# Performance work log

Hardware: AMD Instinct MI355X
Metric: run time of the kernel (lower is better)

## Reference

```python
import jax, jax.numpy as jnp
import numpy as np

K = 9
VOCAB = 7
DIM = 512
LOW = 256  # downsampled bottleneck dim
N_LAYERS = 2
EPS = 1e-5


def _inorm(x, g, b):
    # InstanceNorm1d over length axis (biased var), x: (N, C, K)
    m = jnp.mean(x, axis=-1, keepdims=True)
    v = jnp.mean((x - m) ** 2, axis=-1, keepdims=True)
    return g[None, :, None] * (x - m) * jax.lax.rsqrt(v + EPS) + b[None, :, None]


def _conv5_same(x, w, b):
    # x: (N, C, K), w: (O, C, 5), dilation 1, padding 'same' -> pad 2
    y = jax.lax.conv_general_dilated(
        x, w, window_strides=(1,), padding=[(2, 2)],
        dimension_numbers=('NCH', 'OIH', 'NCH'))
    return y + b[None, :, None]


def _bytenet_layer(x, p):
    (g1, b1, g2, b2, g3, b3, w1, c1b, w2, c2b, w3, c3b) = p
    h = jax.nn.gelu(_inorm(x, g1, b1), approximate=False)
    h = jnp.einsum('nck,oc->nok', h, w1) + c1b[None, :, None]      # 1x1 conv 512->256
    h = jax.nn.gelu(_inorm(h, g2, b2), approximate=False)
    h = _conv5_same(h, w2, c2b)                                     # k=5 conv 256->256
    h = jax.nn.gelu(_inorm(h, g3, b3), approximate=False)
    h = jnp.einsum('nck,oc->nok', h, w3) + c3b[None, :, None]      # 1x1 conv 256->512
    return h + x  # dropout is identity in eval


def setup_inputs() -> dict:
    key = jax.random.key(0)
    ks = jax.random.split(key, 16)
    x = jax.random.randint(ks[0], (8, 2048), 0, VOCAB)
    emb = jax.random.normal(ks[1], (VOCAB, DIM), jnp.float32) * 0.02
    emb = emb.at[6].set(0.0)  # padding_idx=6
    d = {
        'x': x,
        'emb': emb,
        'ln1_w': jnp.ones((N_LAYERS, DIM)), 'ln1_b': jnp.zeros((N_LAYERS, DIM)),
        'ln2_w': jnp.ones((N_LAYERS, LOW)), 'ln2_b': jnp.zeros((N_LAYERS, LOW)),
        'ln3_w': jnp.ones((N_LAYERS, LOW)), 'ln3_b': jnp.zeros((N_LAYERS, LOW)),
        'c1_w': jax.random.normal(ks[2], (N_LAYERS, LOW, DIM), jnp.float32) * 0.02,
        'c1_b': jnp.zeros((N_LAYERS, LOW)),
        'c2_w': jax.random.normal(ks[3], (N_LAYERS, LOW, LOW, 5), jnp.float32) * 0.02,
        'c2_b': jnp.zeros((N_LAYERS, LOW)),
        'c3_w': jax.random.normal(ks[4], (N_LAYERS, DIM, LOW), jnp.float32) * 0.02,
        'c3_b': jnp.zeros((N_LAYERS, DIM)),
        'out_w': jax.random.normal(ks[5], (VOCAB, DIM * K), jnp.float32) * 0.02,
        'out_b': jnp.zeros((VOCAB,)),
    }
    return d


def reference(x, emb, ln1_w, ln1_b, ln2_w, ln2_b, ln3_w, ln3_b,
              c1_w, c1_b, c2_w, c2_b, c3_w, c3_b, out_w, out_b):
    B, L = x.shape
    W = L - K + 1
    e = emb[x]                                        # (B, L, D)
    idx = jnp.arange(W)[:, None] + jnp.arange(K)      # (W, K)
    win = e[:, idx, :]                                # (B, W, K, D)
    h = win.transpose(0, 1, 3, 2).reshape(B * W, DIM, K)  # (N, D, K)
    for i in range(N_LAYERS):
        p = (ln1_w[i], ln1_b[i], ln2_w[i], ln2_b[i], ln3_w[i], ln3_b[i],
             c1_w[i], c1_b[i], c2_w[i], c2_b[i], c3_w[i], c3_b[i])
        h = _bytenet_layer(h, p)
    pred = h.reshape(B * W, DIM * K) @ out_w.T + out_b
    return pred.reshape(B, W, VOCAB)
```

## Files before the change

kernel.cpp:

```cpp
#include <hip/hip_runtime.h>

typedef __attribute__((ext_vector_type(8))) short bfv8;
typedef __attribute__((ext_vector_type(4))) float f32x4;
typedef __attribute__((ext_vector_type(4))) unsigned short usv4;

typedef __attribute__((address_space(1))) const void gvoid;
typedef __attribute__((address_space(3))) void lvoid;
__device__ __forceinline__ void gload16(const void* g, void* l) {
  __builtin_amdgcn_global_load_lds((gvoid*)g, (lvoid*)l, 16, 0, 0);
}

__device__ __forceinline__ float bf2f(unsigned short u) {
  union { unsigned int i; float f; } c; c.i = ((unsigned int)u) << 16; return c.f;
}
__device__ __forceinline__ unsigned short f2bf(float f) {
  union { float f; unsigned int i; } c; c.f = f;
  unsigned int r = c.i + 0x7FFFu + ((c.i >> 16) & 1u);
  return (unsigned short)(r >> 16);
}
__device__ __forceinline__ float gelu_(float x) {
  float z2 = 1.5957691216057308f * x * __builtin_fmaf(0.044715f, x * x, 1.0f);
  float e = __expf(z2);
  float t = __builtin_amdgcn_rcpf(e + 1.0f);
  return x - x * t;
}
__device__ __forceinline__ int div9(int col) {
  return (int)(__umulhi((unsigned)col, 954437177u) >> 1);
}

#define CHP 132
#define CHP2 66

__global__ void k_prep(const float* c1w, const float* c2w, const float* c3w,
                       const float* outw, unsigned short* W1b, unsigned short* W2t,
                       unsigned short* W3b, float* OWt) {
  int i = blockIdx.x * 256 + threadIdx.x;
  if (i < 262144) { W1b[i] = f2bf(c1w[i]); return; }
  i -= 262144;
  if (i < 655360) {
    int ii = i & 255, o = (i >> 8) & 255, rest = i >> 16;
    int t = rest % 5, l = rest / 5;
    W2t[i] = f2bf(c2w[(((l * 256 + o) << 8) + ii) * 5 + t]);
    return;
  }
  i -= 655360;
  if (i < 262144) { W3b[i] = f2bf(c3w[i]); return; }
  i -= 262144;
  if (i < 32256) {
    int c = i & 511, rk = i >> 9;
    int r = rk / 9, k = rk - 9 * r;
    OWt[i] = outw[r * 4608 + c * 9 + k];
  }
}

__global__ void k_x0(const int* x, const float* emb, unsigned short* X, int n0) {
  int idx = blockIdx.x * 256 + threadIdx.x;
  int c4 = idx & 127, nl = idx >> 7;
  int gn = n0 + nl, b = gn >> 11, w = gn & 2047;
  unsigned short* dst = X + (size_t)(12 + nl * 12) * 512 + (c4 << 2);
  const int* xb = x + (b << 11);
  #pragma unroll
  for (int k = 0; k < 9; k++) {
    int t = w + k; if (t > 2047) t = 2047;
    const float* e = emb + xb[t] * 512 + (c4 << 2);
    float4 ev = *(const float4*)e;
    usv4 pk;
    pk[0] = f2bf(ev.x); pk[1] = f2bf(ev.y);
    pk[2] = f2bf(ev.z); pk[3] = f2bf(ev.w);
    *(usv4*)(dst + k * 512) = pk;
  }
}

__global__ void k_zpad(unsigned short* AL) {
  int i = threadIdx.x;
  for (; i < 12 * 256; i += 256) AL[i] = 0;
}

template <int MODE>
__global__ __launch_bounds__(512, 2) void k_gemm(
    const unsigned short* __restrict__ Aw, const unsigned short* __restrict__ Bsrc,
    const float* __restrict__ n1w, const float* __restrict__ n1b,
    const float* __restrict__ gw, const float* __restrict__ gb,
    unsigned short* __restrict__ Out, int nkc) {
  __shared__ __align__(16) unsigned short smem[69632];
  unsigned short* sE = smem;

  const int KROW = (MODE == 0) ? 512 : 256;
  const int KSTEPS = (MODE == 1) ? 20 : 8;
  int tid = threadIdx.x, wv = tid >> 6, ln = tid & 63;
  int lr = ln >> 3, lu = ln & 7;
  int swz = (lu ^ lr) << 3;
  int w0 = blockIdx.x << 5;
  int col0 = blockIdx.x * 288;

  int brow[5];
  #pragma unroll
  for (int s = 0; s < 5; s++) {
    int colg = col0 + (s << 6) + (wv << 3) + lr;
    if (colg >= nkc) colg = nkc - 1;
    brow[s] = colg + 3 * div9(colg) + 12;
  }

  f32x4 acc[4][9];
  #pragma unroll
  for (int i = 0; i < 4; i++)
    #pragma unroll
    for (int j = 0; j < 9; j++) acc[i][j] = (f32x4){0.f, 0.f, 0.f, 0.f};

  auto stage = [&](int buf, int ks) {
    int kb, dlt; const unsigned short* Ab;
    if (MODE == 1) {
      int t = ks % 5; kb = (ks / 5) << 6; dlt = t - 2; Ab = Aw + t * 65536;
    } else { kb = ks << 6; dlt = 0; Ab = Aw; }
    unsigned short* cA = smem + buf * 16384;
    unsigned short* cB = smem + 32768 + buf * 18432;
    #pragma unroll
    for (int p = 0; p < 4; p++) {
      int m = (p << 6) + (wv << 3) + lr;
      gload16(Ab + (size_t)m * KROW + kb + swz, cA + (p << 12) + (wv << 9));
    }
    #pragma unroll
    for (int s = 0; s < 4; s++)
      gload16(Bsrc + (size_t)(brow[s] + dlt) * KROW + kb + swz,
              cB + (s << 12) + (wv << 9));
    if (wv < 4)
      gload16(Bsrc + (size_t)(brow[4] + dlt) * KROW + kb + swz,
              cB + (4 << 12) + (wv << 9));
  };

  stage(0, 0);
  __syncthreads();

  int cur = 0;
  for (int ks = 0; ks < KSTEPS; ks++) {
    unsigned short* cA = smem + cur * 16384;
    unsigned short* cB = smem + 32768 + cur * 18432;

    if (MODE == 0) {
      int cg = tid & 15, win = tid >> 4;
      int u = cg >> 1, sub = (cg & 1) << 3;
      int gch = (ks << 6) + (cg << 2);
      float v[9][4], s1[4] = {0.f, 0.f, 0.f, 0.f};
      #pragma unroll
      for (int k = 0; k < 9; k++) {
        int cl = win * 9 + k;
        usv4 rv = *(const usv4*)((char*)cB + cl * 128 + ((u ^ (cl & 7)) << 4) + sub);
        #pragma unroll
        for (int j = 0; j < 4; j++) { v[k][j] = bf2f(rv[j]); s1[j] += v[k][j]; }
      }
      float mn[4], rr[4], gg[4], bo[4];
      #pragma unroll
      for (int j = 0; j < 4; j++) {
        mn[j] = s1[j] * (1.0f / 9.0f);
        float q = 0.f;
        #pragma unroll
        for (int k = 0; k < 9; k++) { float d = v[k][j] - mn[j]; q += d * d; }
        rr[j] = rsqrtf(q * (1.0f / 9.0f) + 1e-5f);
        gg[j] = n1w[gch + j]; bo[j] = n1b[gch + j];
      }
      #pragma unroll
      for (int k = 0; k < 9; k++) {
        int cl = win * 9 + k;
        usv4 pk;
        #pragma unroll
        for (int j = 0; j < 4; j++)
          pk[j] = f2bf(gelu_(gg[j] * (v[k][j] - mn[j]) * rr[j] + bo[j]));
        *(usv4*)((char*)cB + cl * 128 + ((u ^ (cl & 7)) << 4) + sub) = pk;
      }
      __syncthreads();
    }

    if (ks + 1 < KSTEPS) stage(cur ^ 1, ks + 1);

    int l16 = ln & 15, loct = ln >> 4;
    int wm = wv >> 1, wn = wv & 1;
    #pragma unroll
    for (int kk = 0; kk < 2; kk++) {
      int kbyte = (kk << 6) + (loct << 4);
      bfv8 af[4], bf_[9];
      #pragma unroll
      for (int mi = 0; mi < 4; mi++) {
        int row = (wm << 6) + (mi << 4) + l16;
        af[mi] = *(const bfv8*)((const char*)cA + row * 128 + (kbyte ^ ((row & 7) << 4)));
      }
      #pragma unroll
      for (int ni = 0; ni < 9; ni++) {
        int row = wn * 144 + (ni << 4) + l16;
        bf_[ni] = *(const bfv8*)((const char*)cB + row * 128 + (kbyte ^ ((row & 7) << 4)));
      }
      #pragma unroll
      for (int mi = 0; mi < 4; mi++)
        #pragma unroll
        for (int ni = 0; ni < 9; ni++)
          acc[mi][ni] = __builtin_amdgcn_mfma_f32_16x16x32_bf16(
              af[mi], bf_[ni], acc[mi][ni], 0, 0, 0);
    }
    __syncthreads();
    cur ^= 1;
  }

  int l16 = ln & 15, loct = ln >> 4;
  #pragma unroll
  for (int R = 0; R < 2; R++) {
    if (R) __syncthreads();
    if ((wv >> 2) == R) {
      int chh = (((wv >> 1) & 1) << 6) + (loct << 2);
      int colb = (wv & 1) * 144 + l16;
      #pragma unroll
      for (int mi = 0; mi < 4; mi++) {
        #pragma unroll
        for (int ni = 0; ni < 9; ni++) {
          usv4 pk;
          #pragma unroll
          for (int q = 0; q < 4; q++) pk[q] = f2bf(acc[mi][ni][q]);
          *(usv4*)(sE + (colb + (ni << 4)) * CHP + chh + (mi << 4)) = pk;
        }
      }
    }
    __syncthreads();
    #pragma unroll
    for (int tt = 0; tt < 2; tt++) {
      int t = tid + tt * 512;
      int c4 = t & 31, win = t >> 5;
      int chl = (R << 7) + (c4 << 2);
      const unsigned short* sb = sE + (win * 9) * CHP + (c4 << 2);
      size_t ob = (size_t)(12 + (size_t)(w0 + win) * 12) * 256 + chl;
      float s1[4] = {0.f, 0.f, 0.f, 0.f}, s2[4] = {0.f, 0.f, 0.f, 0.f};
      #pragma unroll
      for (int k = 0; k < 9; k++) {
        usv4 rv = *(const usv4*)(sb + k * CHP);
        #pragma unroll
        for (int j = 0; j < 4; j++) {
          float f = bf2f(rv[j]);
          s1[j] += f; s2[j] = __builtin_fmaf(f, f, s2[j]);
        }
      }
      float mn[4], rr[4], gg[4], bo[4];
      #pragma unroll
      for (int j = 0; j < 4; j++) {
        mn[j] = s1[j] * (1.0f / 9.0f);
        float var = s2[j] * (1.0f / 9.0f) - mn[j] * mn[j];
        rr[j] = rsqrtf(var + 1e-5f);
        gg[j] = gw[chl + j]; bo[j] = gb[chl + j];
      }
      #pragma unroll
      for (int k = 0; k < 9; k++) {
        usv4 rv = *(const usv4*)(sb + k * CHP);
        usv4 pk;
        #pragma unroll
        for (int j = 0; j < 4; j++)
          pk[j] = f2bf(gelu_(gg[j] * (bf2f(rv[j]) - mn[j]) * rr[j] + bo[j]));
        *(usv4*)(Out + ob + k * 256) = pk;
      }
      if (MODE == 0) {
        usv4 z = (usv4){0, 0, 0, 0};
        *(usv4*)(Out + ob + 9 * 256) = z;
        *(usv4*)(Out + ob + 10 * 256) = z;
        *(usv4*)(Out + ob + 11 * 256) = z;
      }
    }
  }
}

__global__ __launch_bounds__(256, 2) void k_gemm2(
    const unsigned short* __restrict__ Aw, const unsigned short* __restrict__ Bsrc,
    const float* __restrict__ cbias, unsigned short* __restrict__ Out, int nkc) {
  __shared__ __align__(16) unsigned short smem[34816];
  unsigned short* sE = smem;

  const int KROW = 256, KSTEPS = 4;
  int tid = threadIdx.x, wv = tid >> 6, ln = tid & 63;
  int lr = ln >> 3, lu = ln & 7;
  int swz = (lu ^ lr) << 3;
  int id = blockIdx.x;
  int slab = (id >> 3) & 3;
  int tile = ((id >> 5) << 3) | (id & 7);
  int m0 = slab << 7;
  int w0 = tile << 4;
  int col0 = tile * 144;

  int brow[5];
  #pragma unroll
  for (int s = 0; s < 5; s++) {
    int cl = (s < 4) ? ((s << 5) + (wv << 3) + lr) : (128 + (wv << 3) + lr);
    int colg = col0 + cl;
    if (colg >= nkc) colg = nkc - 1;
    brow[s] = colg + 3 * div9(colg) + 12;
  }
  const unsigned short* A0 = Aw + (size_t)m0 * KROW;

  f32x4 acc[2][9];
  #pragma unroll
  for (int i = 0; i < 2; i++)
    #pragma unroll
    for (int j = 0; j < 9; j++) acc[i][j] = (f32x4){0.f, 0.f, 0.f, 0.f};

  auto stage = [&](int buf, int ks) {
    int kb = ks << 6;
    unsigned short* cA = smem + buf * 8192;
    unsigned short* cB = smem + 16384 + buf * 9216;
    #pragma unroll
    for (int p = 0; p < 4; p++) {
      int m = (p << 5) + (wv << 3) + lr;
      gload16(A0 + (size_t)m * KROW + kb + swz, cA + ((p << 5) + (wv << 3)) * 64);
    }
    #pragma unroll
    for (int s = 0; s < 4; s++)
      gload16(Bsrc + (size_t)brow[s] * KROW + kb + swz,
              cB + ((s << 5) + (wv << 3)) * 64);
    if (wv < 2)
      gload16(Bsrc + (size_t)brow[4] * KROW + kb + swz,
              cB + (128 + (wv << 3)) * 64);
  };

  stage(0, 0);
  __syncthreads();

  int cur = 0;
  for (int ks = 0; ks < KSTEPS; ks++) {
    unsigned short* cA = smem + cur * 8192;
    unsigned short* cB = smem + 16384 + cur * 9216;
    if (ks + 1 < KSTEPS) stage(cur ^ 1, ks + 1);

    int l16 = ln & 15, loct = ln >> 4;
    #pragma unroll
    for (int kk = 0; kk < 2; kk++) {
      int kbyte = (kk << 6) + (loct << 4);
      bfv8 af[2], bf_[9];
      #pragma unroll
      for (int mi = 0; mi < 2; mi++) {
        int row = (wv << 5) + (mi << 4) + l16;
        af[mi] = *(const bfv8*)((const char*)cA + row * 128 + (kbyte ^ ((row & 7) << 4)));
      }
      #pragma unroll
      for (int ni = 0; ni < 9; ni++) {
        int row = (ni << 4) + l16;
        bf_[ni] = *(const bfv8*)((const char*)cB + row * 128 + (kbyte ^ ((row & 7) << 4)));
      }
      #pragma unroll
      for (int mi = 0; mi < 2; mi++)
        #pragma unroll
        for (int ni = 0; ni < 9; ni++)
          acc[mi][ni] = __builtin_amdgcn_mfma_f32_16x16x32_bf16(
              af[mi], bf_[ni], acc[mi][ni], 0, 0, 0);
    }
    __syncthreads();
    cur ^= 1;
  }

  int l16 = ln & 15, loct = ln >> 4;
  int c4 = tid & 15, win = tid >> 4;
  #pragma unroll
  for (int R = 0; R < 2; R++) {
    if (R) __syncthreads();
    if ((wv >> 1) == R) {
      int chh = ((wv & 1) << 5) + (loct << 2);
      #pragma unroll
      for (int mi = 0; mi < 2; mi++) {
        #pragma unroll
        for (int ni = 0; ni < 9; ni++) {
          usv4 pk;
          #pragma unroll
          for (int q = 0; q < 4; q++) pk[q] = f2bf(acc[mi][ni][q]);
          *(usv4*)(sE + ((ni << 4) + l16) * CHP2 + chh + (mi << 4)) = pk;
        }
      }
    }
    __syncthreads();
    {
      int chg = m0 + (R << 6) + (c4 << 2);
      const unsigned short* sb = sE + (win * 9) * CHP2 + (c4 << 2);
      size_t ob = (size_t)(12 + (size_t)(w0 + win) * 12) * 512 + chg;
      float cb[4];
      #pragma unroll
      for (int j = 0; j < 4; j++) cb[j] = cbias[chg + j];
      #pragma unroll
      for (int k = 0; k < 9; k++) {
        usv4 rv = *(const usv4*)(sb + k * CHP2);
        usv4 old = *(usv4*)(Out + ob + k * 512);
        usv4 pk;
        #pragma unroll
        for (int j = 0; j < 4; j++)
          pk[j] = f2bf(bf2f(rv[j]) + cb[j] + bf2f(old[j]));
        *(usv4*)(Out + ob + k * 512) = pk;
      }
    }
  }
}

__global__ void k_out(const unsigned short* X, const float* OWt, const float* outb,
                      float* pred, int n0, int nc) {
  int gw = (blockIdx.x * 256 + threadIdx.x) >> 6;
  int ln = threadIdx.x & 63;
  if (gw >= nc) return;
  int gn = n0 + gw, b = gn >> 11, w = gn & 2047;
  if (w >= 2040) return;
  const unsigned short* xb = X + (size_t)(12 + gw * 12) * 512 + ln * 8;
  float a[7];
  #pragma unroll
  for (int r = 0; r < 7; r++) a[r] = 0.f;
  for (int k = 0; k < 9; k++) {
    bfv8 xv = *(const bfv8*)(xb + k * 512);
    float xf[8];
    #pragma unroll
    for (int j = 0; j < 8; j++) xf[j] = bf2f((unsigned short)xv[j]);
    #pragma unroll
    for (int r = 0; r < 7; r++) {
      const float* wp = OWt + (r * 9 + k) * 512 + ln * 8;
      float4 w0 = *(const float4*)(wp);
      float4 w1 = *(const float4*)(wp + 4);
      a[r] += xf[0] * w0.x + xf[1] * w0.y + xf[2] * w0.z + xf[3] * w0.w +
              xf[4] * w1.x + xf[5] * w1.y + xf[6] * w1.z + xf[7] * w1.w;
    }
  }
  #pragma unroll
  for (int r = 0; r < 7; r++)
    for (int off = 32; off; off >>= 1) a[r] += __shfl_down(a[r], off);
  if (ln == 0) {
    float* o = pred + (size_t)(b * 2040 + w) * 7;
    #pragma unroll
    for (int r = 0; r < 7; r++) o[r] = a[r] + outb[r];
  }
}

extern "C" void kernel_launch(void* const* d_in, const int* in_sizes, int n_in,
                              void* d_out, int out_size, void* d_ws, size_t ws_size,
                              hipStream_t stream) {
  const int*   x    = (const int*)d_in[0];
  const float* emb  = (const float*)d_in[1];
  const float* ln1w = (const float*)d_in[2];
  const float* ln1b = (const float*)d_in[3];
  const float* ln2w = (const float*)d_in[4];
  const float* ln2b = (const float*)d_in[5];
  const float* ln3w = (const float*)d_in[6];
  const float* ln3b = (const float*)d_in[7];
  const float* c1w  = (const float*)d_in[8];
  const float* c2w  = (const float*)d_in[10];
  const float* c3w  = (const float*)d_in[12];
  const float* c3b  = (const float*)d_in[13];
  const float* outw = (const float*)d_in[14];
  const float* outb = (const float*)d_in[15];
  float* pred = (float*)d_out;

  int nc = 8192;
  while (nc > 128 &&
         2488320ull + (unsigned long long)(nc + 1) * 24576ull > ws_size)
    nc >>= 1;
  int nkc = nc * 9;
  int tiles288 = nc >> 5;
  int tiles144 = nc >> 4;
  int nchunks = 16384 / nc;

  char* ws = (char*)d_ws;
  unsigned short* W1b = (unsigned short*)(ws);
  unsigned short* W2t = (unsigned short*)(ws + 524288);
  unsigned short* W3b = (unsigned short*)(ws + 1835008);
  float*          OWt = (float*)(ws + 2359296);
  char* act = ws + 2488320;
  size_t hiB = (size_t)(nc + 1) * 12288;
  size_t loB = (size_t)(nc + 1) * 6144;
  unsigned short* X   = (unsigned short*)(act);
  unsigned short* AL  = (unsigned short*)(act + hiB);
  unsigned short* AL2 = (unsigned short*)(act + hiB + loB);

  k_prep<<<(1211904 + 255) / 256, 256, 0, stream>>>(c1w, c2w, c3w, outw,
                                                    W1b, W2t, W3b, OWt);
  k_zpad<<<1, 256, 0, stream>>>(AL);

  for (int ch = 0; ch < nchunks; ch++) {
    int n0 = ch * nc;
    k_x0<<<nc / 2, 256, 0, stream>>>(x, emb, X, n0);
    for (int l = 0; l < 2; l++) {
      k_gemm<0><<<dim3(tiles288, 1), 512, 0, stream>>>(
          W1b + l * 131072, X, ln1w + l * 512, ln1b + l * 512,
          ln2w + l * 256, ln2b + l * 256, AL, nkc);
      k_gemm<1><<<dim3(tiles288, 1), 512, 0, stream>>>(
          W2t + l * 327680, AL, nullptr, nullptr,
          ln3w + l * 256, ln3b + l * 256, AL2, nkc);
      k_gemm2<<<tiles144 * 4, 256, 0, stream>>>(
          W3b + l * 131072, AL2, c3b + l * 512, X, nkc);
    }
    k_out<<<nc / 4, 256, 0, stream>>>(X, OWt, outb, pred, n0, nc);
  }
}
```

Measured before the change: 774.5 us.

## Move first-norm GELU out of GEMM into producer epilogues writing a separate buffer

The instance-norm plus GELU on the 512-channel input is no longer done inside the first 1x1-conv GEMM's k-loop. It is now done once by the producer: the embedding kernel for layer 0, and the residual epilogue of the previous layer's output GEMM for layer 1. The results go to a new bf16 buffer T. This removes an extra __syncthreads and ALU work per k-step from the GEMM, and the norm statistics now come from fp32 values rather than bf16-rounded ones. In exchange it writes and reads an extra full-width activation buffer, and the larger workspace can shrink the chunk size.

```diff
diff --git a/kernel.cpp b/kernel.cpp
--- a/kernel.cpp
+++ b/kernel.cpp
@@ -53,21 +53,42 @@
   }
 }
 
-__global__ void k_x0(const int* x, const float* emb, unsigned short* X, int n0) {
+__global__ void k_xng(const int* x, const float* emb, const float* g,
+                      const float* bb, unsigned short* X, unsigned short* T,
+                      int n0) {
   int idx = blockIdx.x * 256 + threadIdx.x;
   int c4 = idx & 127, nl = idx >> 7;
   int gn = n0 + nl, b = gn >> 11, w = gn & 2047;
-  unsigned short* dst = X + (size_t)(12 + nl * 12) * 512 + (c4 << 2);
+  size_t rbase = (size_t)(12 + nl * 12) * 512 + (c4 << 2);
   const int* xb = x + (b << 11);
+  float v[9][4], s1[4] = {0.f, 0.f, 0.f, 0.f};
   #pragma unroll
   for (int k = 0; k < 9; k++) {
     int t = w + k; if (t > 2047) t = 2047;
-    const float* e = emb + xb[t] * 512 + (c4 << 2);
-    float4 ev = *(const float4*)e;
+    float4 ev = *(const float4*)(emb + xb[t] * 512 + (c4 << 2));
+    v[k][0] = ev.x; v[k][1] = ev.y; v[k][2] = ev.z; v[k][3] = ev.w;
     usv4 pk;
-    pk[0] = f2bf(ev.x); pk[1] = f2bf(ev.y);
-    pk[2] = f2bf(ev.z); pk[3] = f2bf(ev.w);
-    *(usv4*)(dst + k * 512) = pk;
+    #pragma unroll
+    for (int j = 0; j < 4; j++) { pk[j] = f2bf(v[k][j]); s1[j] += v[k][j]; }
+    *(usv4*)(X + rbase + k * 512) = pk;
+  }
+  float mn[4], rr[4], gg[4], bo[4];
+  #pragma unroll
+  for (int j = 0; j < 4; j++) {
+    mn[j] = s1[j] * (1.0f / 9.0f);
+    float q = 0.f;
+    #pragma unroll
+    for (int k = 0; k < 9; k++) { float d = v[k][j] - mn[j]; q += d * d; }
+    rr[j] = rsqrtf(q * (1.0f / 9.0f) + 1e-5f);
+    gg[j] = g[(c4 << 2) + j]; bo[j] = bb[(c4 << 2) + j];
+  }
+  #pragma unroll
+  for (int k = 0; k < 9; k++) {
+    usv4 pk;
+    #pragma unroll
+    for (int j = 0; j < 4; j++)
+      pk[j] = f2bf(gelu_(gg[j] * (v[k][j] - mn[j]) * rr[j] + bo[j]));
+    *(usv4*)(T + rbase + k * 512) = pk;
   }
 }
 
@@ -79,7 +100,6 @@
 template <int MODE>
 __global__ __launch_bounds__(512, 2) void k_gemm(
     const unsigned short* __restrict__ Aw, const unsigned short* __restrict__ Bsrc,
-    const float* __restrict__ n1w, const float* __restrict__ n1b,
     const float* __restrict__ gw, const float* __restrict__ gb,
     unsigned short* __restrict__ Out, int nkc) {
   __shared__ __align__(16) unsigned short smem[69632];
@@ -136,40 +156,6 @@
     unsigned short* cA = smem + cur * 16384;
     unsigned short* cB = smem + 32768 + cur * 18432;
 
-    if (MODE == 0) {
-      int cg = tid & 15, win = tid >> 4;
-      int u = cg >> 1, sub = (cg & 1) << 3;
-      int gch = (ks << 6) + (cg << 2);
-      float v[9][4], s1[4] = {0.f, 0.f, 0.f, 0.f};
-      #pragma unroll
-      for (int k = 0; k < 9; k++) {
-        int cl = win * 9 + k;
-        usv4 rv = *(const usv4*)((char*)cB + cl * 128 + ((u ^ (cl & 7)) << 4) + sub);
-        #pragma unroll
-        for (int j = 0; j < 4; j++) { v[k][j] = bf2f(rv[j]); s1[j] += v[k][j]; }
-      }
-      float mn[4], rr[4], gg[4], bo[4];
-      #pragma unroll
-      for (int j = 0; j < 4; j++) {
-        mn[j] = s1[j] * (1.0f / 9.0f);
-        float q = 0.f;
-        #pragma unroll
-        for (int k = 0; k < 9; k++) { float d = v[k][j] - mn[j]; q += d * d; }
-        rr[j] = rsqrtf(q * (1.0f / 9.0f) + 1e-5f);
-        gg[j] = n1w[gch + j]; bo[j] = n1b[gch + j];
-      }
-      #pragma unroll
-      for (int k = 0; k < 9; k++) {
-        int cl = win * 9 + k;
-        usv4 pk;
-        #pragma unroll
-        for (int j = 0; j < 4; j++)
-          pk[j] = f2bf(gelu_(gg[j] * (v[k][j] - mn[j]) * rr[j] + bo[j]));
-        *(usv4*)((char*)cB + cl * 128 + ((u ^ (cl & 7)) << 4) + sub) = pk;
-      }
-      __syncthreads();
-    }
-
     if (ks + 1 < KSTEPS) stage(cur ^ 1, ks + 1);
 
     int l16 = ln & 15, loct = ln >> 4;
@@ -262,9 +248,12 @@
   }
 }
 
+template <bool WT>
 __global__ __launch_bounds__(256, 2) void k_gemm2(
     const unsigned short* __restrict__ Aw, const unsigned short* __restrict__ Bsrc,
-    const float* __restrict__ cbias, unsigned short* __restrict__ Out, int nkc) {
+    const float* __restrict__ cbias, const float* __restrict__ n1w,
+    const float* __restrict__ n1b, unsigned short* __restrict__ Out,
+    unsigned short* __restrict__ Tout, int nkc) {
   __shared__ __align__(16) unsigned short smem[34816];
   unsigned short* sE = smem;
 
@@ -374,15 +363,39 @@
       float cb[4];
       #pragma unroll
       for (int j = 0; j < 4; j++) cb[j] = cbias[chg + j];
+      float v[9][4], s1[4] = {0.f, 0.f, 0.f, 0.f};
       #pragma unroll
       for (int k = 0; k < 9; k++) {
         usv4 rv = *(const usv4*)(sb + k * CHP2);
         usv4 old = *(usv4*)(Out + ob + k * 512);
         usv4 pk;
         #pragma unroll
-        for (int j = 0; j < 4; j++)
-          pk[j] = f2bf(bf2f(rv[j]) + cb[j] + bf2f(old[j]));
+        for (int j = 0; j < 4; j++) {
+          float f = bf2f(rv[j]) + cb[j] + bf2f(old[j]);
+          v[k][j] = f; s1[j] += f;
+          pk[j] = f2bf(f);
+        }
         *(usv4*)(Out + ob + k * 512) = pk;
+      }
+      if (WT) {
+        float mn[4], rr[4], gg[4], bo[4];
+        #pragma unroll
+        for (int j = 0; j < 4; j++) {
+          mn[j] = s1[j] * (1.0f / 9.0f);
+          float q = 0.f;
+          #pragma unroll
+          for (int k = 0; k < 9; k++) { float d = v[k][j] - mn[j]; q += d * d; }
+          rr[j] = rsqrtf(q * (1.0f / 9.0f) + 1e-5f);
+          gg[j] = n1w[chg + j]; bo[j] = n1b[chg + j];
+        }
+        #pragma unroll
+        for (int k = 0; k < 9; k++) {
+          usv4 pk;
+          #pragma unroll
+          for (int j = 0; j < 4; j++)
+            pk[j] = f2bf(gelu_(gg[j] * (v[k][j] - mn[j]) * rr[j] + bo[j]));
+          *(usv4*)(Tout + ob + k * 512) = pk;
+        }
       }
     }
   }
@@ -444,7 +457,7 @@
 
   int nc = 8192;
   while (nc > 128 &&
-         2488320ull + (unsigned long long)(nc + 1) * 24576ull > ws_size)
+         2488320ull + (unsigned long long)(nc + 1) * 36864ull > ws_size)
     nc >>= 1;
   int nkc = nc * 9;
   int tiles288 = nc >> 5;
@@ -460,8 +473,9 @@
   size_t hiB = (size_t)(nc + 1) * 12288;
   size_t loB = (size_t)(nc + 1) * 6144;
   unsigned short* X   = (unsigned short*)(act);
-  unsigned short* AL  = (unsigned short*)(act + hiB);
-  unsigned short* AL2 = (unsigned short*)(act + hiB + loB);
+  unsigned short* T   = (unsigned short*)(act + hiB);
+  unsigned short* AL  = (unsigned short*)(act + 2 * hiB);
+  unsigned short* AL2 = (unsigned short*)(act + 2 * hiB + loB);
 
   k_prep<<<(1211904 + 255) / 256, 256, 0, stream>>>(c1w, c2w, c3w, outw,
                                                     W1b, W2t, W3b, OWt);
@@ -469,16 +483,18 @@
 
   for (int ch = 0; ch < nchunks; ch++) {
     int n0 = ch * nc;
-    k_x0<<<nc / 2, 256, 0, stream>>>(x, emb, X, n0);
+    k_xng<<<nc / 2, 256, 0, stream>>>(x, emb, ln1w, ln1b, X, T, n0);
     for (int l = 0; l < 2; l++) {
       k_gemm<0><<<dim3(tiles288, 1), 512, 0, stream>>>(
-          W1b + l * 131072, X, ln1w + l * 512, ln1b + l * 512,
-          ln2w + l * 256, ln2b + l * 256, AL, nkc);
+          W1b + l * 131072, T, ln2w + l * 256, ln2b + l * 256, AL, nkc);
       k_gemm<1><<<dim3(tiles288, 1), 512, 0, stream>>>(
-          W2t + l * 327680, AL, nullptr, nullptr,
-          ln3w + l * 256, ln3b + l * 256, AL2, nkc);
-      k_gemm2<<<tiles144 * 4, 256, 0, stream>>>(
-          W3b + l * 131072, AL2, c3b + l * 512, X, nkc);
+          W2t + l * 327680, AL, ln3w + l * 256, ln3b + l * 256, AL2, nkc);
+      if (l == 0)
+        k_gemm2<true><<<tiles144 * 4, 256, 0, stream>>>(
+            W3b, AL2, c3b, ln1w + 512, ln1b + 512, X, T, nkc);
+      else
+        k_gemm2<false><<<tiles144 * 4, 256, 0, stream>>>(
+            W3b + 131072, AL2, c3b + 512, nullptr, nullptr, X, nullptr, nkc);
     }
     k_out<<<nc / 4, 256, 0, stream>>>(X, OWt, outb, pred, n0, nc);
   }
```

Measured after the change: 1.045 ms. +34.9%, slower.

## Fuse output projection into last layer's GEMM epilogue with atomic accumulation

Applied to the files above, without the earlier changes.

The final 7-way output projection is folded into the epilogue of the second layer's 256->512 GEMM. The fp32 residual sum is dotted with the output weights in registers, reduced across lanes with shuffles, and accumulated into pred with atomicAdd. pred is pre-initialised with the bias by a new kernel. This drops the separate k_out launch and the bf16 write-back and re-read of X for the last layer, but adds atomics from the four channel slabs per window and extra register pressure in the epilogue.

```diff
diff --git a/kernel.cpp b/kernel.cpp
--- a/kernel.cpp
+++ b/kernel.cpp
@@ -53,6 +53,11 @@
   }
 }
 
+__global__ void k_pinit(const float* outb, float* pred) {
+  int i = blockIdx.x * 256 + threadIdx.x;
+  if (i < 114240) pred[i] = outb[i % 7];
+}
+
 __global__ void k_x0(const int* x, const float* emb, unsigned short* X, int n0) {
   int idx = blockIdx.x * 256 + threadIdx.x;
   int c4 = idx & 127, nl = idx >> 7;
@@ -262,9 +267,11 @@
   }
 }
 
+template <bool FOUT>
 __global__ __launch_bounds__(256, 2) void k_gemm2(
     const unsigned short* __restrict__ Aw, const unsigned short* __restrict__ Bsrc,
-    const float* __restrict__ cbias, unsigned short* __restrict__ Out, int nkc) {
+    const float* __restrict__ cbias, unsigned short* __restrict__ Out, int nkc,
+    const float* __restrict__ OWt, float* __restrict__ pred, int n0) {
   __shared__ __align__(16) unsigned short smem[34816];
   unsigned short* sE = smem;
 
@@ -374,52 +381,49 @@
       float cb[4];
       #pragma unroll
       for (int j = 0; j < 4; j++) cb[j] = cbias[chg + j];
-      #pragma unroll
-      for (int k = 0; k < 9; k++) {
-        usv4 rv = *(const usv4*)(sb + k * CHP2);
-        usv4 old = *(usv4*)(Out + ob + k * 512);
-        usv4 pk;
-        #pragma unroll
-        for (int j = 0; j < 4; j++)
-          pk[j] = f2bf(bf2f(rv[j]) + cb[j] + bf2f(old[j]));
-        *(usv4*)(Out + ob + k * 512) = pk;
-      }
-    }
-  }
-}
-
-__global__ void k_out(const unsigned short* X, const float* OWt, const float* outb,
-                      float* pred, int n0, int nc) {
-  int gw = (blockIdx.x * 256 + threadIdx.x) >> 6;
-  int ln = threadIdx.x & 63;
-  if (gw >= nc) return;
-  int gn = n0 + gw, b = gn >> 11, w = gn & 2047;
-  if (w >= 2040) return;
-  const unsigned short* xb = X + (size_t)(12 + gw * 12) * 512 + ln * 8;
-  float a[7];
-  #pragma unroll
-  for (int r = 0; r < 7; r++) a[r] = 0.f;
-  for (int k = 0; k < 9; k++) {
-    bfv8 xv = *(const bfv8*)(xb + k * 512);
-    float xf[8];
-    #pragma unroll
-    for (int j = 0; j < 8; j++) xf[j] = bf2f((unsigned short)xv[j]);
-    #pragma unroll
-    for (int r = 0; r < 7; r++) {
-      const float* wp = OWt + (r * 9 + k) * 512 + ln * 8;
-      float4 w0 = *(const float4*)(wp);
-      float4 w1 = *(const float4*)(wp + 4);
-      a[r] += xf[0] * w0.x + xf[1] * w0.y + xf[2] * w0.z + xf[3] * w0.w +
-              xf[4] * w1.x + xf[5] * w1.y + xf[6] * w1.z + xf[7] * w1.w;
-    }
-  }
-  #pragma unroll
-  for (int r = 0; r < 7; r++)
-    for (int off = 32; off; off >>= 1) a[r] += __shfl_down(a[r], off);
-  if (ln == 0) {
-    float* o = pred + (size_t)(b * 2040 + w) * 7;
-    #pragma unroll
-    for (int r = 0; r < 7; r++) o[r] = a[r] + outb[r];
+      if (!FOUT) {
+        #pragma unroll
+        for (int k = 0; k < 9; k++) {
+          usv4 rv = *(const usv4*)(sb + k * CHP2);
+          usv4 old = *(usv4*)(Out + ob + k * 512);
+          usv4 pk;
+          #pragma unroll
+          for (int j = 0; j < 4; j++)
+            pk[j] = f2bf(bf2f(rv[j]) + cb[j] + bf2f(old[j]));
+          *(usv4*)(Out + ob + k * 512) = pk;
+        }
+      } else {
+        float v[9][4];
+        #pragma unroll
+        for (int k = 0; k < 9; k++) {
+          usv4 rv = *(const usv4*)(sb + k * CHP2);
+          usv4 old = *(usv4*)(Out + ob + k * 512);
+          #pragma unroll
+          for (int j = 0; j < 4; j++)
+            v[k][j] = bf2f(rv[j]) + cb[j] + bf2f(old[j]);
+        }
+        int gn = n0 + w0 + win, b = gn >> 11, w = gn & 2047;
+        #pragma unroll
+        for (int r = 0; r < 7; r++) {
+          float p = 0.f;
+          #pragma unroll
+          for (int k = 0; k < 9; k++) {
+            const float* wp = OWt + (r * 9 + k) * 512 + chg;
+            float4 wvv = *(const float4*)wp;
+            p = __builtin_fmaf(v[k][0], wvv.x, p);
+            p = __builtin_fmaf(v[k][1], wvv.y, p);
+            p = __builtin_fmaf(v[k][2], wvv.z, p);
+            p = __builtin_fmaf(v[k][3], wvv.w, p);
+          }
+          p += __shfl_xor(p, 1);
+          p += __shfl_xor(p, 2);
+          p += __shfl_xor(p, 4);
+          p += __shfl_xor(p, 8);
+          if (c4 == 0 && w < 2040)
+            atomicAdd(pred + (size_t)(b * 2040 + w) * 7 + r, p);
+        }
+      }
+    }
   }
 }
 
@@ -466,6 +470,7 @@
   k_prep<<<(1211904 + 255) / 256, 256, 0, stream>>>(c1w, c2w, c3w, outw,
                                                     W1b, W2t, W3b, OWt);
   k_zpad<<<1, 256, 0, stream>>>(AL);
+  k_pinit<<<(114240 + 255) / 256, 256, 0, stream>>>(outb, pred);
 
   for (int ch = 0; ch < nchunks; ch++) {
     int n0 = ch * nc;
@@ -477,9 +482,12 @@
       k_gemm<1><<<dim3(tiles288, 1), 512, 0, stream>>>(
           W2t + l * 327680, AL, nullptr, nullptr,
           ln3w + l * 256, ln3b + l * 256, AL2, nkc);
-      k_gemm2<<<tiles144 * 4, 256, 0, stream>>>(
-          W3b + l * 131072, AL2, c3b + l * 512, X, nkc);
-    }
-    k_out<<<nc / 4, 256, 0, stream>>>(X, OWt, outb, pred, n0, nc);
-  }
-}
+      if (l == 0)
+        k_gemm2<false><<<tiles144 * 4, 256, 0, stream>>>(
+            W3b, AL2, c3b, X, nkc, nullptr, nullptr, 0);
+      else
+        k_gemm2<true><<<tiles144 * 4, 256, 0, stream>>>(
+            W3b + 131072, AL2, c3b + 512, X, nkc, OWt, pred, n0);
+    }
+  }
+}
```

New measurement: 757.4 us. 2.2% less time.
